# Kernel optimization log

Measured on AMD Instinct MI355X. Metric: run time of the kernel, lower is better.

The kernel has to match this reference:

```python
import jax, jax.numpy as jnp
import numpy as np

NUM_NODES = 100000
NUM_EDGES = 1600000
D = 128

def sage_conv(x, src, dst, Wl, bl, Wr):
    # PyG SAGEConv (mean aggr): out = lin_l(mean_{j->i} x_j) + lin_r(x_i)
    msgs = x[src]                                            # [E, D] gather
    agg = jax.ops.segment_sum(msgs, dst, num_segments=x.shape[0])  # [N, D]
    deg = jax.ops.segment_sum(jnp.ones((src.shape[0],), x.dtype), dst,
                              num_segments=x.shape[0])       # [N]
    mean = agg / jnp.maximum(deg, 1.0)[:, None]
    return mean @ Wl.T + bl + x @ Wr.T

def setup_inputs() -> dict:
    key = jax.random.key(0)
    ks = jax.random.split(key, 16)
    s = 1.0 / np.sqrt(D)
    inp = {
        'x': jax.random.randint(ks[0], (NUM_NODES, 1), 0, NUM_NODES),
        'edge_index': jax.random.randint(ks[1], (2, NUM_EDGES), 0, NUM_NODES),
        'batch': jnp.zeros((NUM_NODES,), dtype=jnp.int64),
        'item_emb': jax.random.normal(ks[2], (NUM_NODES, D), jnp.float32),
        'edge_emb': jax.random.normal(ks[3], (NUM_EDGES, D), jnp.float32),
        'Wl1': jax.random.uniform(ks[4], (D, D), jnp.float32, -s, s),
        'bl1': jnp.zeros((D,), jnp.float32),
        'Wr1': jax.random.uniform(ks[5], (D, D), jnp.float32, -s, s),
        'Wl2': jax.random.uniform(ks[6], (D, D), jnp.float32, -s, s),
        'bl2': jnp.zeros((D,), jnp.float32),
        'Wr2': jax.random.uniform(ks[7], (D, D), jnp.float32, -s, s),
        'Wl3': jax.random.uniform(ks[8], (D, D), jnp.float32, -s, s),
        'bl3': jnp.zeros((D,), jnp.float32),
        'Wr3': jax.random.uniform(ks[9], (D, D), jnp.float32, -s, s),
        'W_lin1': jax.random.uniform(ks[10], (D, D), jnp.float32, -s, s),
        'b_lin1': jnp.zeros((D,), jnp.float32),
        'W_lin2': jax.random.uniform(ks[11], (D, D), jnp.float32, -s, s),
        'b_lin2': jnp.zeros((D,), jnp.float32),
    }
    return inp

def reference(x, edge_index, batch, item_emb, edge_emb,
              Wl1, bl1, Wr1, Wl2, bl2, Wr2, Wl3, bl3, Wr3,
              W_lin1, b_lin1, W_lin2, b_lin2):
    src, dst = edge_index[0], edge_index[1]
    h = item_emb[x[:, 0]]                      # embedding lookup + squeeze(1) -> [N, D]
    e = edge_emb                               # edge_embedding(arange(E)) == full table
    h = jax.nn.relu(sage_conv(h, src, dst, Wl1, bl1, Wr1))
    h = jax.nn.relu(sage_conv(h, src, dst, Wl2, bl2, Wr2))
    h = jax.nn.relu(sage_conv(h, src, dst, Wl3, bl3, Wr3))
    h = jax.nn.relu(h @ W_lin1.T + b_lin1)     # dropout is identity in eval mode
    e_out = jax.nn.relu(e @ W_lin2.T + b_lin2)
    return h, e_out
```

## Files before the change

kernel.cpp:

```cpp
#include <hip/hip_runtime.h>

#define NN  100000
#define NNP 100096
#define NE  1600000
#define DD  128

typedef __attribute__((ext_vector_type(8))) short bf16x8;
typedef __attribute__((ext_vector_type(4))) float f32x4;

__device__ __forceinline__ float bf2f(unsigned short u){
  union { unsigned int i; float f; } v; v.i = ((unsigned int)u) << 16; return v.f;
}
__device__ __forceinline__ unsigned short f2bf(float f){
  union { float f; unsigned int i; } v; v.f = f;
  unsigned int u = v.i;
  return (unsigned short)((u + 0x7fffu + ((u >> 16) & 1u)) >> 16);
}
__device__ __forceinline__ unsigned int cvt_pk_bf16(float lo, float hi){
  unsigned int r;
  asm("v_cvt_pk_bf16_f32 %0, %1, %2" : "=v"(r) : "v"(lo), "v"(hi));
  return r;
}

struct WPtrs { const float* w[8]; };
__global__ __launch_bounds__(256) void cvt_w_all(WPtrs wp, unsigned short* __restrict__ o){
  int t = blockIdx.x * 256 + threadIdx.x;
  int m = t >> 13, i = t & 8191;
  float2 v = ((const float2*)wp.w[m])[i];
  ((unsigned int*)o)[t] = cvt_pk_bf16(v.x, v.y);
}

__global__ __launch_bounds__(256) void count_deg(const int* __restrict__ dst,
                                                 int* __restrict__ deg, int n){
  int t = blockIdx.x * 256 + threadIdx.x;
  if (t < n) atomicAdd(&deg[dst[t]], 1);
}

#define SCAN_CHUNK 1024
__global__ __launch_bounds__(256) void partial_sums(const int* __restrict__ deg,
                                                    int* __restrict__ partials, int n){
  __shared__ int lds[256];
  int t = threadIdx.x;
  int base = blockIdx.x * SCAN_CHUNK + t * 4;
  int s = 0;
  #pragma unroll
  for (int i = 0; i < 4; ++i){ int idx = base + i; s += (idx < n) ? deg[idx] : 0; }
  lds[t] = s; __syncthreads();
  for (int off = 128; off > 0; off >>= 1){
    if (t < off) lds[t] += lds[t + off];
    __syncthreads();
  }
  if (t == 0) partials[blockIdx.x] = lds[0];
}

__global__ void scan_partials(int* partials, int nb){
  if (threadIdx.x == 0 && blockIdx.x == 0){
    int acc = 0;
    for (int i = 0; i < nb; ++i){ int v = partials[i]; partials[i] = acc; acc += v; }
  }
}

__global__ __launch_bounds__(256) void scan_block(const int* __restrict__ deg,
                                                  const int* __restrict__ partials,
                                                  int* __restrict__ row_start, int n){
  __shared__ int lds[256];
  int t = threadIdx.x;
  int base = blockIdx.x * SCAN_CHUNK + t * 4;
  int v[4]; int s = 0;
  #pragma unroll
  for (int i = 0; i < 4; ++i){ int idx = base + i; v[i] = (idx < n) ? deg[idx] : 0; s += v[i]; }
  lds[t] = s; __syncthreads();
  for (int off = 1; off < 256; off <<= 1){
    int x = (t >= off) ? lds[t - off] : 0;
    __syncthreads();
    lds[t] += x;
    __syncthreads();
  }
  int excl = ((t == 0) ? 0 : lds[t - 1]) + partials[blockIdx.x];
  #pragma unroll
  for (int i = 0; i < 4; ++i){ int idx = base + i; if (idx < n) row_start[idx] = excl; excl += v[i]; }
}

__global__ __launch_bounds__(256) void fill_csr(const int* __restrict__ src,
                                                const int* __restrict__ dst,
                                                const int* __restrict__ row_start,
                                                int* __restrict__ cursor,
                                                int* __restrict__ csr, int n){
  int t = blockIdx.x * 256 + threadIdx.x;
  if (t < n){
    int d = dst[t];
    int pos = atomicAdd(&cursor[d], 1);
    csr[row_start[d] + pos] = src[t];
  }
}

__global__ __launch_bounds__(256) void gather_h0(const int* __restrict__ x,
                                                 const float* __restrict__ emb,
                                                 unsigned short* __restrict__ h, int n){
  int t = blockIdx.x * 256 + threadIdx.x;
  if (t >= n * 64) return;
  int node = t >> 6, p = t & 63;
  int s = x[node];
  float2 v = *(const float2*)(emb + (size_t)s * DD + p * 2);
  ((unsigned int*)h)[t] = cvt_pk_bf16(v.x, v.y);
}

__global__ __launch_bounds__(256) void aggregate3(const unsigned short* __restrict__ h,
                                                  const int* __restrict__ csr,
                                                  const int* __restrict__ row_start,
                                                  const int* __restrict__ deg,
                                                  unsigned short* __restrict__ mean, int n){
  int node = blockIdx.x * 4 + (threadIdx.x >> 6);
  int lane = threadIdx.x & 63;
  int st = __builtin_amdgcn_readfirstlane(row_start[node]);
  int d  = __builtin_amdgcn_readfirstlane(deg[node]);
  const unsigned int* hp = (const unsigned int*)h;
  float a0[8], a1[8];
  #pragma unroll
  for (int k = 0; k < 8; ++k){ a0[k] = 0.f; a1[k] = 0.f; }
  int i = 0;
  for (; i + 8 <= d; i += 8){
    int idx[8];
    #pragma unroll
    for (int k = 0; k < 8; ++k) idx[k] = csr[st + i + k];
    unsigned int v[8];
    #pragma unroll
    for (int k = 0; k < 8; ++k) v[k] = hp[(size_t)idx[k] * 64 + lane];
    #pragma unroll
    for (int k = 0; k < 8; ++k){
      a0[k] += bf2f((unsigned short)(v[k] & 0xffffu));
      a1[k] += bf2f((unsigned short)(v[k] >> 16));
    }
  }
  for (; i + 4 <= d; i += 4){
    int idx[4];
    #pragma unroll
    for (int k = 0; k < 4; ++k) idx[k] = csr[st + i + k];
    unsigned int v[4];
    #pragma unroll
    for (int k = 0; k < 4; ++k) v[k] = hp[(size_t)idx[k] * 64 + lane];
    #pragma unroll
    for (int k = 0; k < 4; ++k){
      a0[k] += bf2f((unsigned short)(v[k] & 0xffffu));
      a1[k] += bf2f((unsigned short)(v[k] >> 16));
    }
  }
  for (; i < d; ++i){
    int s = csr[st + i];
    unsigned int v = hp[(size_t)s * 64 + lane];
    a0[0] += bf2f((unsigned short)(v & 0xffffu));
    a1[0] += bf2f((unsigned short)(v >> 16));
  }
  float s0 = ((a0[0] + a0[1]) + (a0[2] + a0[3])) + ((a0[4] + a0[5]) + (a0[6] + a0[7]));
  float s1 = ((a1[0] + a1[1]) + (a1[2] + a1[3])) + ((a1[4] + a1[5]) + (a1[6] + a1[7]));
  float inv = 1.0f / fmaxf((float)d, 1.0f);
  ((unsigned int*)mean)[(size_t)node * 64 + lane] = cvt_pk_bf16(s0 * inv, s1 * inv);
}

__device__ __forceinline__ void stage_mat(const unsigned short* __restrict__ Bg,
                                          unsigned short* sB){
  int t = threadIdx.x;
  #pragma unroll
  for (int it = 0; it < 8; ++it){
    int idx = it * 256 + t;
    int kc = idx >> 7, col = idx & 127;
    uint4 v = *(const uint4*)(Bg + (size_t)col * DD + kc * 8);
    *(uint4*)(sB + (size_t)idx * 8) = v;
  }
}

__global__ __launch_bounds__(256) void gemm_edge3(
    const float* __restrict__ A, const unsigned short* __restrict__ Bg,
    const float* __restrict__ bias, float* __restrict__ out)
{
  __shared__ unsigned short sB[16384];
  stage_mat(Bg, sB);
  int wave = threadIdx.x >> 6, lane = threadIdx.x & 63;
  int lr = lane & 15, lk = lane >> 4;
  size_t r0 = (size_t)blockIdx.x * 128 + (size_t)wave * 32;
  const float* Ap = A + (r0 + lr) * DD + lk * 8;

  f32x4 raw[2][4][2];
  #pragma unroll
  for (int g = 0; g < 2; ++g)
    #pragma unroll
    for (int ks = 0; ks < 4; ++ks){
      raw[g][ks][0] = __builtin_nontemporal_load((const f32x4*)(Ap + (size_t)g * 16 * DD + ks * 32));
      raw[g][ks][1] = __builtin_nontemporal_load((const f32x4*)(Ap + (size_t)g * 16 * DD + ks * 32 + 4));
    }
  float bv[8];
  #pragma unroll
  for (int j = 0; j < 8; ++j) bv[j] = bias[j * 16 + lr];

  __syncthreads();

  bf16x8 a[2][4];
  #pragma unroll
  for (int g = 0; g < 2; ++g)
    #pragma unroll
    for (int ks = 0; ks < 4; ++ks){
      union { bf16x8 v; unsigned int u[4]; } au;
      au.u[0] = cvt_pk_bf16(raw[g][ks][0][0], raw[g][ks][0][1]);
      au.u[1] = cvt_pk_bf16(raw[g][ks][0][2], raw[g][ks][0][3]);
      au.u[2] = cvt_pk_bf16(raw[g][ks][1][0], raw[g][ks][1][1]);
      au.u[3] = cvt_pk_bf16(raw[g][ks][1][2], raw[g][ks][1][3]);
      a[g][ks] = au.v;
    }

  f32x4 acc[2][8];
  #pragma unroll
  for (int g = 0; g < 2; ++g)
    #pragma unroll
    for (int j = 0; j < 8; ++j) acc[g][j] = (f32x4){0.f, 0.f, 0.f, 0.f};
  #pragma unroll
  for (int ks = 0; ks < 4; ++ks){
    #pragma unroll
    for (int j = 0; j < 8; ++j){
      bf16x8 b = *(const bf16x8*)(sB + ((ks * 4 + lk) * 128 + j * 16 + lr) * 8);
      acc[0][j] = __builtin_amdgcn_mfma_f32_16x16x32_bf16(a[0][ks], b, acc[0][j], 0, 0, 0);
      acc[1][j] = __builtin_amdgcn_mfma_f32_16x16x32_bf16(a[1][ks], b, acc[1][j], 0, 0, 0);
    }
  }
  #pragma unroll
  for (int g = 0; g < 2; ++g)
    #pragma unroll
    for (int j = 0; j < 8; ++j)
      #pragma unroll
      for (int r = 0; r < 4; ++r){
        size_t row = r0 + g * 16 + lk * 4 + r;
        __builtin_nontemporal_store(fmaxf(acc[g][j][r] + bv[j], 0.f),
                                    &out[row * DD + j * 16 + lr]);
      }
}

template<int DUAL, int OUTF32>
__global__ __launch_bounds__(256) void gemm_node2(
    const unsigned short* __restrict__ A1, const unsigned short* __restrict__ B1g,
    const unsigned short* __restrict__ A2, const unsigned short* __restrict__ B2g,
    const float* __restrict__ bias, void* __restrict__ outp, int M, int ntiles)
{
  __shared__ unsigned short sB[DUAL ? 32768 : 16384];
  stage_mat(B1g, sB);
  if (DUAL) stage_mat(B2g, sB + 16384);
  __syncthreads();
  int wave = threadIdx.x >> 6, lane = threadIdx.x & 63;
  int lr = lane & 15, lk = lane >> 4;
  float bv[8];
  #pragma unroll
  for (int j = 0; j < 8; ++j) bv[j] = bias[j * 16 + lr];

  for (int tile = blockIdx.x; tile < ntiles; tile += gridDim.x){
    size_t r0 = (size_t)tile * 128 + wave * 32;
    f32x4 acc[2][8];
    #pragma unroll
    for (int g = 0; g < 2; ++g)
      #pragma unroll
      for (int j = 0; j < 8; ++j) acc[g][j] = (f32x4){0.f, 0.f, 0.f, 0.f};

    {
      const unsigned short* Ap = A1 + (r0 + lr) * DD + lk * 8;
      bf16x8 a[2][4];
      #pragma unroll
      for (int g = 0; g < 2; ++g)
        #pragma unroll
        for (int ks = 0; ks < 4; ++ks)
          a[g][ks] = *(const bf16x8*)(Ap + (size_t)g * 16 * DD + ks * 32);
      #pragma unroll
      for (int ks = 0; ks < 4; ++ks){
        #pragma unroll
        for (int j = 0; j < 8; ++j){
          bf16x8 b = *(const bf16x8*)(sB + ((ks * 4 + lk) * 128 + j * 16 + lr) * 8);
          acc[0][j] = __builtin_amdgcn_mfma_f32_16x16x32_bf16(a[0][ks], b, acc[0][j], 0, 0, 0);
          acc[1][j] = __builtin_amdgcn_mfma_f32_16x16x32_bf16(a[1][ks], b, acc[1][j], 0, 0, 0);
        }
      }
    }
    if (DUAL){
      const unsigned short* Ap = A2 + (r0 + lr) * DD + lk * 8;
      bf16x8 a[2][4];
      #pragma unroll
      for (int g = 0; g < 2; ++g)
        #pragma unroll
        for (int ks = 0; ks < 4; ++ks)
          a[g][ks] = *(const bf16x8*)(Ap + (size_t)g * 16 * DD + ks * 32);
      #pragma unroll
      for (int ks = 0; ks < 4; ++ks){
        #pragma unroll
        for (int j = 0; j < 8; ++j){
          bf16x8 b = *(const bf16x8*)(sB + 16384 + ((ks * 4 + lk) * 128 + j * 16 + lr) * 8);
          acc[0][j] = __builtin_amdgcn_mfma_f32_16x16x32_bf16(a[0][ks], b, acc[0][j], 0, 0, 0);
          acc[1][j] = __builtin_amdgcn_mfma_f32_16x16x32_bf16(a[1][ks], b, acc[1][j], 0, 0, 0);
        }
      }
    }
    #pragma unroll
    for (int g = 0; g < 2; ++g)
      #pragma unroll
      for (int j = 0; j < 8; ++j)
        #pragma unroll
        for (int r = 0; r < 4; ++r){
          size_t row = r0 + g * 16 + lk * 4 + r;
          float v = fmaxf(acc[g][j][r] + bv[j], 0.f);
          if (OUTF32){
            if (row < (size_t)M)
              __builtin_nontemporal_store(v, ((float*)outp) + row * DD + j * 16 + lr);
          } else {
            ((unsigned short*)outp)[row * DD + j * 16 + lr] = f2bf(v);
          }
        }
  }
}

extern "C" void kernel_launch(void* const* d_in, const int* in_sizes, int n_in,
                              void* d_out, int out_size, void* d_ws, size_t ws_size,
                              hipStream_t stream)
{
  const int*   x    = (const int*)d_in[0];
  const int*   ei   = (const int*)d_in[1];
  const int*   srcp = ei;
  const int*   dstp = ei + NE;
  const float* item = (const float*)d_in[3];
  const float* eemb = (const float*)d_in[4];
  WPtrs wp;
  wp.w[0] = (const float*)d_in[5];
  wp.w[1] = (const float*)d_in[7];
  wp.w[2] = (const float*)d_in[8];
  wp.w[3] = (const float*)d_in[10];
  wp.w[4] = (const float*)d_in[11];
  wp.w[5] = (const float*)d_in[13];
  wp.w[6] = (const float*)d_in[14];
  wp.w[7] = (const float*)d_in[16];
  const float* bl1 = (const float*)d_in[6];
  const float* bl2 = (const float*)d_in[9];
  const float* bl3 = (const float*)d_in[12];
  const float* bq1 = (const float*)d_in[15];
  const float* bq2 = (const float*)d_in[17];

  char* ws = (char*)d_ws;
  size_t o = 0;
  auto alloc = [&](size_t bytes) -> void* {
    void* p = ws + o;
    o += (bytes + 255) & ~(size_t)255;
    return p;
  };
  unsigned short* wbf      = (unsigned short*)alloc(8 * 16384 * 2);
  int*            deg      = (int*)alloc((size_t)NN * 4);
  int*            cursor   = (int*)alloc((size_t)NN * 4);
  int*            row_st   = (int*)alloc((size_t)NN * 4);
  int*            partials = (int*)alloc(4096);
  int*            csr      = (int*)alloc((size_t)NE * 4);
  unsigned short* mean     = (unsigned short*)alloc((size_t)NNP * DD * 2);
  unsigned short* h_a      = (unsigned short*)alloc((size_t)NNP * DD * 2);
  unsigned short* h_b      = (unsigned short*)alloc((size_t)NNP * DD * 2);

  float* out_h = (float*)d_out;
  float* out_e = out_h + (size_t)NN * DD;

  hipMemsetAsync(deg, 0, (((size_t)NN * 4 + 255) & ~(size_t)255) * 2, stream);

  cvt_w_all<<<256, 256, 0, stream>>>(wp, wbf);

  const int nb = (NN + SCAN_CHUNK - 1) / SCAN_CHUNK;
  count_deg<<<(NE + 255) / 256, 256, 0, stream>>>(dstp, deg, NE);
  partial_sums<<<nb, 256, 0, stream>>>(deg, partials, NN);
  scan_partials<<<1, 64, 0, stream>>>(partials, nb);
  scan_block<<<nb, 256, 0, stream>>>(deg, partials, row_st, NN);
  fill_csr<<<(NE + 255) / 256, 256, 0, stream>>>(srcp, dstp, row_st, cursor, csr, NE);

  gather_h0<<<(NN * 64 + 255) / 256, 256, 0, stream>>>(x, item, h_a, NN);

  const int agg_grid   = (NN + 3) / 4;
  const int node_tiles = NNP / 128;
  const int edge_tiles = NE / 128;

  aggregate3<<<agg_grid, 256, 0, stream>>>(h_a, csr, row_st, deg, mean, NN);
  gemm_node2<1,0><<<node_tiles, 256, 0, stream>>>(mean, wbf + 0*16384, h_a, wbf + 1*16384, bl1, h_b, NN, node_tiles);
  aggregate3<<<agg_grid, 256, 0, stream>>>(h_b, csr, row_st, deg, mean, NN);
  gemm_node2<1,0><<<node_tiles, 256, 0, stream>>>(mean, wbf + 2*16384, h_b, wbf + 3*16384, bl2, h_a, NN, node_tiles);
  aggregate3<<<agg_grid, 256, 0, stream>>>(h_a, csr, row_st, deg, mean, NN);
  gemm_node2<1,0><<<node_tiles, 256, 0, stream>>>(mean, wbf + 4*16384, h_a, wbf + 5*16384, bl3, h_b, NN, node_tiles);

  gemm_node2<0,1><<<node_tiles, 256, 0, stream>>>(h_b, wbf + 6*16384, h_b, wbf + 6*16384, bq1, out_h, NN, node_tiles);

  gemm_edge3<<<edge_tiles, 256, 0, stream>>>(eemb, wbf + 7*16384, bq2, out_e);
}
```

Baseline: 887.7 us.

## Spread edge-embedding GEMM tiles across CSR, aggregation and node GEMM kernels

Removes the standalone edge GEMM kernel and splits its 25000 tiles of 64 rows across every other launch: degree count, CSR fill, the three aggregations and the four node GEMMs. Extra blocks in each grid run the edge linear layer. The aim is for the bandwidth-heavy edge GEMM to overlap with the latency-bound gather and atomic kernels, filling otherwise idle CUs. The node GEMM is also retiled to 64 rows per block with a single reused 32KB LDS buffer and a launch bound of 4 blocks per CU. In exchange, the LDS footprint of the edge path now sits on all fused kernels, and the nontemporal load and store hints on the node and edge outputs are dropped.

```diff
diff --git a/kernel.cpp b/kernel.cpp
--- a/kernel.cpp
+++ b/kernel.cpp
@@ -30,10 +30,97 @@
   ((unsigned int*)o)[t] = cvt_pk_bf16(v.x, v.y);
 }
 
-__global__ __launch_bounds__(256) void count_deg(const int* __restrict__ dst,
-                                                 int* __restrict__ deg, int n){
+__device__ __forceinline__ void stage_mat(const unsigned short* __restrict__ Bg,
+                                          unsigned short* sB){
+  int t = threadIdx.x;
+  #pragma unroll
+  for (int it = 0; it < 8; ++it){
+    int idx = it * 256 + t;
+    int kc = idx >> 7, col = idx & 127;
+    uint4 v = *(const uint4*)(Bg + (size_t)col * DD + kc * 8);
+    *(uint4*)(sB + (size_t)idx * 8) = v;
+  }
+}
+
+__device__ __forceinline__ void edge_body(int tile, const float* __restrict__ A,
+    const unsigned short* __restrict__ Wg, const float* __restrict__ bias,
+    float* __restrict__ out, unsigned short* sB)
+{
+  stage_mat(Wg, sB);
+  int w = threadIdx.x >> 6, lane = threadIdx.x & 63;
+  int lr = lane & 15, lk = lane >> 4;
+  size_t r0 = (size_t)tile * 64 + (size_t)w * 16;
+  const float* Ap = A + (r0 + lr) * DD + lk * 8;
+  f32x4 raw[4][2];
+  #pragma unroll
+  for (int ks = 0; ks < 4; ++ks){
+    raw[ks][0] = __builtin_nontemporal_load((const f32x4*)(Ap + ks * 32));
+    raw[ks][1] = __builtin_nontemporal_load((const f32x4*)(Ap + ks * 32 + 4));
+  }
+  float bv[8];
+  #pragma unroll
+  for (int j = 0; j < 8; ++j) bv[j] = bias[j * 16 + lr];
+
+  __syncthreads();
+
+  f32x4 acc[8];
+  #pragma unroll
+  for (int j = 0; j < 8; ++j) acc[j] = (f32x4){0.f, 0.f, 0.f, 0.f};
+  #pragma unroll
+  for (int ks = 0; ks < 4; ++ks){
+    union { bf16x8 v; unsigned int u[4]; } au;
+    au.u[0] = cvt_pk_bf16(raw[ks][0][0], raw[ks][0][1]);
+    au.u[1] = cvt_pk_bf16(raw[ks][0][2], raw[ks][0][3]);
+    au.u[2] = cvt_pk_bf16(raw[ks][1][0], raw[ks][1][1]);
+    au.u[3] = cvt_pk_bf16(raw[ks][1][2], raw[ks][1][3]);
+    #pragma unroll
+    for (int j = 0; j < 8; ++j){
+      bf16x8 b = *(const bf16x8*)(sB + (((ks * 4 + lk) * 128) + j * 16 + lr) * 8);
+      acc[j] = __builtin_amdgcn_mfma_f32_16x16x32_bf16(au.v, b, acc[j], 0, 0, 0);
+    }
+  }
+  #pragma unroll
+  for (int j = 0; j < 8; ++j)
+    #pragma unroll
+    for (int r = 0; r < 4; ++r){
+      size_t row = r0 + lk * 4 + r;
+      out[row * DD + j * 16 + lr] = fmaxf(acc[j][r] + bv[j], 0.f);
+    }
+}
+
+#define EDGE_ARGS const float* __restrict__ eA, const unsigned short* __restrict__ eW, \
+                  const float* __restrict__ eBias, float* __restrict__ eOut, \
+                  int eBase, int eCount
+#define EDGE_PASS eA, eW, eBias, eOut
+
+__global__ __launch_bounds__(256, 4) void countdeg_edge(
+    const int* __restrict__ dst, int* __restrict__ deg, int n, int nblk, EDGE_ARGS){
+  __shared__ unsigned short sB[16384];
+  if ((int)blockIdx.x >= nblk){
+    int e = blockIdx.x - nblk;
+    if (e < eCount) edge_body(eBase + e, EDGE_PASS, sB);
+    return;
+  }
   int t = blockIdx.x * 256 + threadIdx.x;
   if (t < n) atomicAdd(&deg[dst[t]], 1);
+}
+
+__global__ __launch_bounds__(256, 4) void fillcsr_edge(
+    const int* __restrict__ src, const int* __restrict__ dst,
+    const int* __restrict__ row_start, int* __restrict__ cursor,
+    int* __restrict__ csr, int n, int nblk, EDGE_ARGS){
+  __shared__ unsigned short sB[16384];
+  if ((int)blockIdx.x >= nblk){
+    int e = blockIdx.x - nblk;
+    if (e < eCount) edge_body(eBase + e, EDGE_PASS, sB);
+    return;
+  }
+  int t = blockIdx.x * 256 + threadIdx.x;
+  if (t < n){
+    int d = dst[t];
+    int pos = atomicAdd(&cursor[d], 1);
+    csr[row_start[d] + pos] = src[t];
+  }
 }
 
 #define SCAN_CHUNK 1024
@@ -79,19 +166,6 @@
   int excl = ((t == 0) ? 0 : lds[t - 1]) + partials[blockIdx.x];
   #pragma unroll
   for (int i = 0; i < 4; ++i){ int idx = base + i; if (idx < n) row_start[idx] = excl; excl += v[i]; }
-}
-
-__global__ __launch_bounds__(256) void fill_csr(const int* __restrict__ src,
-                                                const int* __restrict__ dst,
-                                                const int* __restrict__ row_start,
-                                                int* __restrict__ cursor,
-                                                int* __restrict__ csr, int n){
-  int t = blockIdx.x * 256 + threadIdx.x;
-  if (t < n){
-    int d = dst[t];
-    int pos = atomicAdd(&cursor[d], 1);
-    csr[row_start[d] + pos] = src[t];
-  }
 }
 
 __global__ __launch_bounds__(256) void gather_h0(const int* __restrict__ x,
@@ -105,12 +179,20 @@
   ((unsigned int*)h)[t] = cvt_pk_bf16(v.x, v.y);
 }
 
-__global__ __launch_bounds__(256) void aggregate3(const unsigned short* __restrict__ h,
-                                                  const int* __restrict__ csr,
-                                                  const int* __restrict__ row_start,
-                                                  const int* __restrict__ deg,
-                                                  unsigned short* __restrict__ mean, int n){
-  int node = blockIdx.x * 4 + (threadIdx.x >> 6);
+__global__ __launch_bounds__(256, 4) void agg_edge(
+    const unsigned short* __restrict__ h,
+    const int* __restrict__ csr, const int* __restrict__ row_start,
+    const int* __restrict__ deg, unsigned short* __restrict__ mean,
+    EDGE_ARGS)
+{
+  __shared__ unsigned short sB[16384];
+  int g = blockIdx.x / 6, r = blockIdx.x % 6;
+  if (r == 5){
+    if (g < eCount) edge_body(eBase + g, EDGE_PASS, sB);
+    return;
+  }
+  int aidx = g * 5 + r;
+  int node = aidx * 4 + (threadIdx.x >> 6);
   int lane = threadIdx.x & 63;
   int st = __builtin_amdgcn_readfirstlane(row_start[node]);
   int d  = __builtin_amdgcn_readfirstlane(deg[node]);
@@ -157,157 +239,71 @@
   ((unsigned int*)mean)[(size_t)node * 64 + lane] = cvt_pk_bf16(s0 * inv, s1 * inv);
 }
 
-__device__ __forceinline__ void stage_mat(const unsigned short* __restrict__ Bg,
-                                          unsigned short* sB){
-  int t = threadIdx.x;
-  #pragma unroll
-  for (int it = 0; it < 8; ++it){
-    int idx = it * 256 + t;
-    int kc = idx >> 7, col = idx & 127;
-    uint4 v = *(const uint4*)(Bg + (size_t)col * DD + kc * 8);
-    *(uint4*)(sB + (size_t)idx * 8) = v;
-  }
-}
-
-__global__ __launch_bounds__(256) void gemm_edge3(
-    const float* __restrict__ A, const unsigned short* __restrict__ Bg,
-    const float* __restrict__ bias, float* __restrict__ out)
+template<int DUAL, int OUTF32>
+__global__ __launch_bounds__(256, 4) void node_edge(
+    const unsigned short* __restrict__ A1, const unsigned short* __restrict__ B1g,
+    const unsigned short* __restrict__ A2, const unsigned short* __restrict__ B2g,
+    const float* __restrict__ bias, void* __restrict__ outp, int n_node,
+    EDGE_ARGS)
 {
   __shared__ unsigned short sB[16384];
-  stage_mat(Bg, sB);
-  int wave = threadIdx.x >> 6, lane = threadIdx.x & 63;
+  if ((int)blockIdx.x >= n_node){
+    int e = blockIdx.x - n_node;
+    if (e < eCount) edge_body(eBase + e, EDGE_PASS, sB);
+    return;
+  }
+  stage_mat(B1g, sB);
+  int w = threadIdx.x >> 6, lane = threadIdx.x & 63;
   int lr = lane & 15, lk = lane >> 4;
-  size_t r0 = (size_t)blockIdx.x * 128 + (size_t)wave * 32;
-  const float* Ap = A + (r0 + lr) * DD + lk * 8;
-
-  f32x4 raw[2][4][2];
-  #pragma unroll
-  for (int g = 0; g < 2; ++g)
+  size_t r0 = (size_t)blockIdx.x * 64 + (size_t)w * 16;
+  float bv[8];
+  #pragma unroll
+  for (int j = 0; j < 8; ++j) bv[j] = bias[j * 16 + lr];
+  f32x4 acc[8];
+  #pragma unroll
+  for (int j = 0; j < 8; ++j) acc[j] = (f32x4){0.f, 0.f, 0.f, 0.f};
+  __syncthreads();
+
+  {
+    const unsigned short* Ap = A1 + (r0 + lr) * DD + lk * 8;
     #pragma unroll
     for (int ks = 0; ks < 4; ++ks){
-      raw[g][ks][0] = __builtin_nontemporal_load((const f32x4*)(Ap + (size_t)g * 16 * DD + ks * 32));
-      raw[g][ks][1] = __builtin_nontemporal_load((const f32x4*)(Ap + (size_t)g * 16 * DD + ks * 32 + 4));
-    }
-  float bv[8];
-  #pragma unroll
-  for (int j = 0; j < 8; ++j) bv[j] = bias[j * 16 + lr];
-
-  __syncthreads();
-
-  bf16x8 a[2][4];
-  #pragma unroll
-  for (int g = 0; g < 2; ++g)
+      bf16x8 a = *(const bf16x8*)(Ap + ks * 32);
+      #pragma unroll
+      for (int j = 0; j < 8; ++j){
+        bf16x8 b = *(const bf16x8*)(sB + (((ks * 4 + lk) * 128) + j * 16 + lr) * 8);
+        acc[j] = __builtin_amdgcn_mfma_f32_16x16x32_bf16(a, b, acc[j], 0, 0, 0);
+      }
+    }
+  }
+  if (DUAL){
+    __syncthreads();
+    stage_mat(B2g, sB);
+    __syncthreads();
+    const unsigned short* Ap = A2 + (r0 + lr) * DD + lk * 8;
     #pragma unroll
     for (int ks = 0; ks < 4; ++ks){
-      union { bf16x8 v; unsigned int u[4]; } au;
-      au.u[0] = cvt_pk_bf16(raw[g][ks][0][0], raw[g][ks][0][1]);
-      au.u[1] = cvt_pk_bf16(raw[g][ks][0][2], raw[g][ks][0][3]);
-      au.u[2] = cvt_pk_bf16(raw[g][ks][1][0], raw[g][ks][1][1]);
-      au.u[3] = cvt_pk_bf16(raw[g][ks][1][2], raw[g][ks][1][3]);
-      a[g][ks] = au.v;
-    }
-
-  f32x4 acc[2][8];
-  #pragma unroll
-  for (int g = 0; g < 2; ++g)
-    #pragma unroll
-    for (int j = 0; j < 8; ++j) acc[g][j] = (f32x4){0.f, 0.f, 0.f, 0.f};
-  #pragma unroll
-  for (int ks = 0; ks < 4; ++ks){
-    #pragma unroll
-    for (int j = 0; j < 8; ++j){
-      bf16x8 b = *(const bf16x8*)(sB + ((ks * 4 + lk) * 128 + j * 16 + lr) * 8);
-      acc[0][j] = __builtin_amdgcn_mfma_f32_16x16x32_bf16(a[0][ks], b, acc[0][j], 0, 0, 0);
-      acc[1][j] = __builtin_amdgcn_mfma_f32_16x16x32_bf16(a[1][ks], b, acc[1][j], 0, 0, 0);
-    }
-  }
-  #pragma unroll
-  for (int g = 0; g < 2; ++g)
-    #pragma unroll
-    for (int j = 0; j < 8; ++j)
+      bf16x8 a = *(const bf16x8*)(Ap + ks * 32);
       #pragma unroll
-      for (int r = 0; r < 4; ++r){
-        size_t row = r0 + g * 16 + lk * 4 + r;
-        __builtin_nontemporal_store(fmaxf(acc[g][j][r] + bv[j], 0.f),
-                                    &out[row * DD + j * 16 + lr]);
+      for (int j = 0; j < 8; ++j){
+        bf16x8 b = *(const bf16x8*)(sB + (((ks * 4 + lk) * 128) + j * 16 + lr) * 8);
+        acc[j] = __builtin_amdgcn_mfma_f32_16x16x32_bf16(a, b, acc[j], 0, 0, 0);
       }
-}
-
-template<int DUAL, int OUTF32>
-__global__ __launch_bounds__(256) void gemm_node2(
-    const unsigned short* __restrict__ A1, const unsigned short* __restrict__ B1g,
-    const unsigned short* __restrict__ A2, const unsigned short* __restrict__ B2g,
-    const float* __restrict__ bias, void* __restrict__ outp, int M, int ntiles)
-{
-  __shared__ unsigned short sB[DUAL ? 32768 : 16384];
-  stage_mat(B1g, sB);
-  if (DUAL) stage_mat(B2g, sB + 16384);
-  __syncthreads();
-  int wave = threadIdx.x >> 6, lane = threadIdx.x & 63;
-  int lr = lane & 15, lk = lane >> 4;
-  float bv[8];
-  #pragma unroll
-  for (int j = 0; j < 8; ++j) bv[j] = bias[j * 16 + lr];
-
-  for (int tile = blockIdx.x; tile < ntiles; tile += gridDim.x){
-    size_t r0 = (size_t)tile * 128 + wave * 32;
-    f32x4 acc[2][8];
-    #pragma unroll
-    for (int g = 0; g < 2; ++g)
-      #pragma unroll
-      for (int j = 0; j < 8; ++j) acc[g][j] = (f32x4){0.f, 0.f, 0.f, 0.f};
-
-    {
-      const unsigned short* Ap = A1 + (r0 + lr) * DD + lk * 8;
-      bf16x8 a[2][4];
-      #pragma unroll
-      for (int g = 0; g < 2; ++g)
-        #pragma unroll
-        for (int ks = 0; ks < 4; ++ks)
-          a[g][ks] = *(const bf16x8*)(Ap + (size_t)g * 16 * DD + ks * 32);
-      #pragma unroll
-      for (int ks = 0; ks < 4; ++ks){
-        #pragma unroll
-        for (int j = 0; j < 8; ++j){
-          bf16x8 b = *(const bf16x8*)(sB + ((ks * 4 + lk) * 128 + j * 16 + lr) * 8);
-          acc[0][j] = __builtin_amdgcn_mfma_f32_16x16x32_bf16(a[0][ks], b, acc[0][j], 0, 0, 0);
-          acc[1][j] = __builtin_amdgcn_mfma_f32_16x16x32_bf16(a[1][ks], b, acc[1][j], 0, 0, 0);
-        }
+    }
+  }
+  #pragma unroll
+  for (int j = 0; j < 8; ++j){
+    int col = j * 16 + lr;
+    #pragma unroll
+    for (int r = 0; r < 4; ++r){
+      size_t row = r0 + lk * 4 + r;
+      float v = fmaxf(acc[j][r] + bv[j], 0.f);
+      if (OUTF32){
+        if (row < (size_t)NN) ((float*)outp)[row * DD + col] = v;
+      } else {
+        ((unsigned short*)outp)[row * DD + col] = f2bf(v);
       }
     }
-    if (DUAL){
-      const unsigned short* Ap = A2 + (r0 + lr) * DD + lk * 8;
-      bf16x8 a[2][4];
-      #pragma unroll
-      for (int g = 0; g < 2; ++g)
-        #pragma unroll
-        for (int ks = 0; ks < 4; ++ks)
-          a[g][ks] = *(const bf16x8*)(Ap + (size_t)g * 16 * DD + ks * 32);
-      #pragma unroll
-      for (int ks = 0; ks < 4; ++ks){
-        #pragma unroll
-        for (int j = 0; j < 8; ++j){
-          bf16x8 b = *(const bf16x8*)(sB + 16384 + ((ks * 4 + lk) * 128 + j * 16 + lr) * 8);
-          acc[0][j] = __builtin_amdgcn_mfma_f32_16x16x32_bf16(a[0][ks], b, acc[0][j], 0, 0, 0);
-          acc[1][j] = __builtin_amdgcn_mfma_f32_16x16x32_bf16(a[1][ks], b, acc[1][j], 0, 0, 0);
-        }
-      }
-    }
-    #pragma unroll
-    for (int g = 0; g < 2; ++g)
-      #pragma unroll
-      for (int j = 0; j < 8; ++j)
-        #pragma unroll
-        for (int r = 0; r < 4; ++r){
-          size_t row = r0 + g * 16 + lk * 4 + r;
-          float v = fmaxf(acc[g][j][r] + bv[j], 0.f);
-          if (OUTF32){
-            if (row < (size_t)M)
-              __builtin_nontemporal_store(v, ((float*)outp) + row * DD + j * 16 + lr);
-          } else {
-            ((unsigned short*)outp)[row * DD + j * 16 + lr] = f2bf(v);
-          }
-        }
   }
 }
 
@@ -344,9 +340,9 @@
     return p;
   };
   unsigned short* wbf      = (unsigned short*)alloc(8 * 16384 * 2);
-  int*            deg      = (int*)alloc((size_t)NN * 4);
-  int*            cursor   = (int*)alloc((size_t)NN * 4);
-  int*            row_st   = (int*)alloc((size_t)NN * 4);
+  int*            deg      = (int*)alloc((size_t)NNP * 4);
+  int*            cursor   = (int*)alloc((size_t)NNP * 4);
+  int*            row_st   = (int*)alloc((size_t)NNP * 4);
   int*            partials = (int*)alloc(4096);
   int*            csr      = (int*)alloc((size_t)NE * 4);
   unsigned short* mean     = (unsigned short*)alloc((size_t)NNP * DD * 2);
@@ -355,32 +351,44 @@
 
   float* out_h = (float*)d_out;
   float* out_e = out_h + (size_t)NN * DD;
-
-  hipMemsetAsync(deg, 0, (((size_t)NN * 4 + 255) & ~(size_t)255) * 2, stream);
+  const unsigned short* eW = wbf + 7 * 16384;
+
+  hipMemsetAsync(deg, 0, (size_t)NNP * 4 * 2, stream);
 
   cvt_w_all<<<256, 256, 0, stream>>>(wp, wbf);
 
+  int eb = 0;
+  const int e_cd = 1250, e_fc = 1250, e_ag = 4500, e_nd = 2500, e_fin = 1500;
+
   const int nb = (NN + SCAN_CHUNK - 1) / SCAN_CHUNK;
-  count_deg<<<(NE + 255) / 256, 256, 0, stream>>>(dstp, deg, NE);
+  const int csr_blk = (NE + 255) / 256;
+
+  countdeg_edge<<<csr_blk + e_cd, 256, 0, stream>>>(dstp, deg, NE, csr_blk,
+      eemb, eW, bq2, out_e, eb, e_cd); eb += e_cd;
   partial_sums<<<nb, 256, 0, stream>>>(deg, partials, NN);
   scan_partials<<<1, 64, 0, stream>>>(partials, nb);
   scan_block<<<nb, 256, 0, stream>>>(deg, partials, row_st, NN);
-  fill_csr<<<(NE + 255) / 256, 256, 0, stream>>>(srcp, dstp, row_st, cursor, csr, NE);
+  fillcsr_edge<<<csr_blk + e_fc, 256, 0, stream>>>(srcp, dstp, row_st, cursor, csr, NE, csr_blk,
+      eemb, eW, bq2, out_e, eb, e_fc); eb += e_fc;
 
   gather_h0<<<(NN * 64 + 255) / 256, 256, 0, stream>>>(x, item, h_a, NN);
 
-  const int agg_grid   = (NN + 3) / 4;
-  const int node_tiles = NNP / 128;
-  const int edge_tiles = NE / 128;
-
-  aggregate3<<<agg_grid, 256, 0, stream>>>(h_a, csr, row_st, deg, mean, NN);
-  gemm_node2<1,0><<<node_tiles, 256, 0, stream>>>(mean, wbf + 0*16384, h_a, wbf + 1*16384, bl1, h_b, NN, node_tiles);
-  aggregate3<<<agg_grid, 256, 0, stream>>>(h_b, csr, row_st, deg, mean, NN);
-  gemm_node2<1,0><<<node_tiles, 256, 0, stream>>>(mean, wbf + 2*16384, h_b, wbf + 3*16384, bl2, h_a, NN, node_tiles);
-  aggregate3<<<agg_grid, 256, 0, stream>>>(h_a, csr, row_st, deg, mean, NN);
-  gemm_node2<1,0><<<node_tiles, 256, 0, stream>>>(mean, wbf + 4*16384, h_a, wbf + 5*16384, bl3, h_b, NN, node_tiles);
-
-  gemm_node2<0,1><<<node_tiles, 256, 0, stream>>>(h_b, wbf + 6*16384, h_b, wbf + 6*16384, bq1, out_h, NN, node_tiles);
-
-  gemm_edge3<<<edge_tiles, 256, 0, stream>>>(eemb, wbf + 7*16384, bq2, out_e);
-}
+  const int node_tiles = NNP / 64;
+  const int agg_grid   = 30000;
+
+  agg_edge<<<agg_grid, 256, 0, stream>>>(h_a, csr, row_st, deg, mean,
+      eemb, eW, bq2, out_e, eb, e_ag); eb += e_ag;
+  node_edge<1,0><<<node_tiles + e_nd, 256, 0, stream>>>(mean, wbf + 0*16384, h_a, wbf + 1*16384,
+      bl1, h_b, node_tiles, eemb, eW, bq2, out_e, eb, e_nd); eb += e_nd;
+  agg_edge<<<agg_grid, 256, 0, stream>>>(h_b, csr, row_st, deg, mean,
+      eemb, eW, bq2, out_e, eb, e_ag); eb += e_ag;
+  node_edge<1,0><<<node_tiles + e_nd, 256, 0, stream>>>(mean, wbf + 2*16384, h_b, wbf + 3*16384,
+      bl2, h_a, node_tiles, eemb, eW, bq2, out_e, eb, e_nd); eb += e_nd;
+  agg_edge<<<agg_grid, 256, 0, stream>>>(h_a, csr, row_st, deg, mean,
+      eemb, eW, bq2, out_e, eb, e_ag); eb += e_ag;
+  node_edge<1,0><<<node_tiles + e_nd, 256, 0, stream>>>(mean, wbf + 4*16384, h_a, wbf + 5*16384,
+      bl3, h_b, node_tiles, eemb, eW, bq2, out_e, eb, e_nd); eb += e_nd;
+
+  node_edge<0,1><<<node_tiles + e_fin, 256, 0, stream>>>(h_b, wbf + 6*16384, h_b, wbf + 6*16384,
+      bq1, out_h, node_tiles, eemb, eW, bq2, out_e, eb, e_fin); eb += e_fin;
+}
```

After: 1.050 ms. 1.18x slower.
